# Performance work log

Hardware: AMD Instinct MI355X
Metric: run time of the kernel (lower is better)

## Reference

```python
import jax, jax.numpy as jnp
import numpy as np

B, S, D, H = 2, 2048, 1024, 16
DK = D // H  # 64


def setup_inputs() -> dict:
    key = jax.random.key(0)
    ks = jax.random.split(key, 9)
    s = 0.02
    return {
        "embeddings": jax.random.normal(ks[0], (B, S, D), jnp.float32),
        "Wq": jax.random.normal(ks[1], (H, D, DK), jnp.float32) * s,
        "bq": jax.random.normal(ks[2], (H, DK), jnp.float32) * s,
        "Wk": jax.random.normal(ks[3], (H, D, DK), jnp.float32) * s,
        "bk": jax.random.normal(ks[4], (H, DK), jnp.float32) * s,
        "Wv": jax.random.normal(ks[5], (H, D, DK), jnp.float32) * s,
        "bv": jax.random.normal(ks[6], (H, DK), jnp.float32) * s,
        "Wo": jax.random.normal(ks[7], (D, D), jnp.float32) * s,
        "bo": jax.random.normal(ks[8], (D,), jnp.float32) * s,
    }


def reference(embeddings, Wq, bq, Wk, bk, Wv, bv, Wo, bo):
    b, s, d = embeddings.shape
    dk = Wq.shape[-1]
    # batched per-head projections: [b,s,d] x [h,d,k] -> [b,h,s,k]
    q = jnp.einsum('bsd,hdk->bhsk', embeddings, Wq) + bq[None, :, None, :]
    k = jnp.einsum('bsd,hdk->bhsk', embeddings, Wk) + bk[None, :, None, :]
    v = jnp.einsum('bsd,hdk->bhsk', embeddings, Wv) + bv[None, :, None, :]
    scores = jnp.einsum('bhqk,bhsk->bhqs', q, k) / jnp.sqrt(jnp.float32(dk))
    causal_mask = jnp.triu(jnp.ones((s, s), dtype=bool), k=1)  # True above diagonal
    scores = jnp.where(causal_mask, jnp.float32(-1e9), scores)
    weights = jax.nn.softmax(scores, axis=-1)
    ctx = jnp.einsum('bhqs,bhsk->bhqk', weights, v)
    concat = ctx.transpose(0, 2, 1, 3).reshape(b, s, d)  # head-major concat, matches torch.cat
    return concat @ Wo + bo
```

## Files before the change

### kernel.cpp

```cpp
#include <hip/hip_runtime.h>
#include <hip/hip_bf16.h>

typedef unsigned short u16;
typedef unsigned int u32;
typedef __bf16 bf16x8 __attribute__((ext_vector_type(8)));
typedef float f32x4 __attribute__((ext_vector_type(4)));
typedef float f32x16 __attribute__((ext_vector_type(16)));

#define AS1 __attribute__((address_space(1)))
#define AS3 __attribute__((address_space(3)))

#define NB 2
#define NS 2048
#define ND 1024
#define NH 16
#define NK 64

__device__ __forceinline__ u16 f2bf(float f) {
  u32 u = __builtin_bit_cast(u32, f);
  return (u16)((u + 0x7FFFu + ((u >> 16) & 1u)) >> 16);
}

__device__ __forceinline__ u32 cvt_pk_bf16(float lo, float hi) {
  u32 u;
  asm("v_cvt_pk_bf16_f32 %0, %1, %2" : "=v"(u) : "v"(lo), "v"(hi));
  return u;
}

__device__ __forceinline__ void stage_tile(u16* lds, const u16* __restrict__ src, int rs,
                                           int wid, int lane) {
#pragma unroll
  for (int i = 0; i < 2; ++i) {
    int c = wid * 128 + i * 64 + lane;
    int row = c >> 3;
    int kc = (c & 7) ^ (row & 7);
    __builtin_amdgcn_global_load_lds((const AS1 u32*)(src + row * rs + kc * 8),
                                     (AS3 u32*)(lds + (wid * 128 + i * 64) * 8), 16, 0, 0);
  }
}

__device__ __forceinline__ bf16x8 read_slot(const u16* lds, int row, int slot) {
  return *(const bf16x8*)(lds + row * 64 + (slot ^ (row & 7)) * 8);
}

__device__ __forceinline__ uint2 ld8(const u16* lds, int row, int col) {
  int slot = (col >> 3) ^ (row & 7);
  return *(const uint2*)(lds + row * 64 + slot * 8 + (col & 7));
}

__device__ __forceinline__ bf16x8 read_vfrag(const u16* lds, int row, int ks, int hi) {
  int c0 = ks * 16 + 4 * hi;
  uint2 a = ld8(lds, row, c0);
  uint2 b = ld8(lds, row, c0 + 8);
  uint4 q; q.x = a.x; q.y = a.y; q.z = b.x; q.w = b.y;
  return __builtin_bit_cast(bf16x8, q);
}

__device__ __forceinline__ bf16x8 read_frag(const u16* lds, int row, int ks, int lane) {
  int slot = ((lane >> 4) + ks * 4) ^ (row & 7);
  return *(const bf16x8*)(lds + row * 64 + slot * 8);
}

__global__ __launch_bounds__(256) void convert_kernel(const float* __restrict__ src,
                                                      u16* __restrict__ dst, int n) {
  int i = (blockIdx.x * 256 + threadIdx.x) * 4;
  if (i >= n) return;
  float4 v = *(const float4*)(src + i);
  u32 w0 = cvt_pk_bf16(v.x, v.y);
  u32 w1 = cvt_pk_bf16(v.z, v.w);
  uint2 w; w.x = w0; w.y = w1;
  *(uint2*)(dst + i) = w;
}

__global__ __launch_bounds__(256) void transpose_conv(const float* __restrict__ src,
                                                      u16* __restrict__ dst, int R, int C) {
  __shared__ float tile[32][33];
  size_t base = (size_t)blockIdx.z * R * C;
  src += base;
  dst += base;
  int c0 = blockIdx.x * 32, r0 = blockIdx.y * 32;
  int tx = threadIdx.x, ty = threadIdx.y;
#pragma unroll
  for (int i = 0; i < 4; ++i)
    tile[ty + 8 * i][tx] = src[(size_t)(r0 + ty + 8 * i) * C + c0 + tx];
  __syncthreads();
#pragma unroll
  for (int i = 0; i < 4; ++i)
    dst[(size_t)(c0 + ty + 8 * i) * R + r0 + tx] = f2bf(tile[tx][ty + 8 * i]);
}

__global__ __launch_bounds__(256) void qkv_kernel(
    const u16* __restrict__ emb, const u16* __restrict__ Wqt, const u16* __restrict__ Wkt,
    const u16* __restrict__ Wvt, const float* __restrict__ bq, const float* __restrict__ bk,
    const float* __restrict__ bv, u16* __restrict__ Q, u16* __restrict__ K,
    u16* __restrict__ Vt) {
  __shared__ alignas(16) u16 lds_a[64 * 64];
  __shared__ alignas(16) u16 lds_b[64 * 64];
  int tid = threadIdx.x, lane = tid & 63, wid = tid >> 6;
  int mt = blockIdx.x, h = blockIdx.y, which = blockIdx.z;
  const u16* Wt = (which == 0 ? Wqt : which == 1 ? Wkt : Wvt) + h * (ND * NK);
  const float* bias = (which == 0 ? bq : which == 1 ? bk : bv) + h * NK;
  int m0 = mt * 64;
  int col = lane & 15;
  f32x4 zero4 = {0.f, 0.f, 0.f, 0.f};
  f32x4 acc[4] = {zero4, zero4, zero4, zero4};
  for (int k0 = 0; k0 < ND; k0 += 64) {
    stage_tile(lds_a, emb + m0 * ND + k0, ND, wid, lane);
    stage_tile(lds_b, Wt + k0, ND, wid, lane);
    __syncthreads();
#pragma unroll
    for (int ks = 0; ks < 2; ++ks) {
      bf16x8 a = read_frag(lds_a, wid * 16 + col, ks, lane);
#pragma unroll
      for (int f = 0; f < 4; ++f) {
        bf16x8 b = read_frag(lds_b, f * 16 + col, ks, lane);
        acc[f] = __builtin_amdgcn_mfma_f32_16x16x32_bf16(a, b, acc[f], 0, 0, 0);
      }
    }
    __syncthreads();
  }
  int rbase = m0 + wid * 16 + (lane >> 4) * 4;
#pragma unroll
  for (int f = 0; f < 4; ++f) {
    int n = f * 16 + col;
    float bn = bias[n];
#pragma unroll
    for (int r = 0; r < 4; ++r) {
      int m = rbase + r;
      int b = m >> 11, s = m & (NS - 1);
      float v = acc[f][r] + bn;
      if (which == 0) {
        Q[((b * NH + h) * NS + s) * NK + n] = f2bf(v * 0.18033688f);
      } else if (which == 1) {
        K[((b * NH + h) * NS + s) * NK + n] = f2bf(v);
      } else {
        Vt[((b * NH + h) * NK + n) * NS + s] = f2bf(v);
      }
    }
  }
}

__global__ __launch_bounds__(256, 2) void attn_kernel(const u16* __restrict__ Q,
                                                      const u16* __restrict__ K,
                                                      const u16* __restrict__ Vt,
                                                      u16* __restrict__ ctx) {
  __shared__ alignas(16) u16 lds_k[2][64 * 64];
  __shared__ alignas(16) u16 lds_v[2][64 * 64];
  __shared__ float slab[4][32];
  int tid = threadIdx.x, lane = tid & 63, w = tid >> 6;
  int hi = lane >> 5, ln = lane & 31;
  int bh = blockIdx.x;
  int y = blockIdx.y;
  int qt = (y < 8) ? (15 - y) : (y - 8);
  const u16* Qb = Q + bh * (NS * NK);
  const u16* Kb = K + bh * (NS * NK);
  const u16* Vb = Vt + bh * (NK * NS);
  int q0w = qt * 128 + w * 32;
  int qg = q0w + ln;
  bf16x8 qf[4];
#pragma unroll
  for (int ks = 0; ks < 4; ++ks)
    qf[ks] = *(const bf16x8*)(Qb + qg * NK + ks * 16 + hi * 8);

  f32x16 acc0, acc1;
#pragma unroll
  for (int r = 0; r < 16; ++r) { acc0[r] = 0.f; acc1[r] = 0.f; }
  float m = -1e30f, lp = 0.f;
  int nt = 2 * qt + 2;
  int tmaxw = (q0w + 31) >> 6;

  stage_tile(lds_k[0], Kb, NK, w, lane);
  stage_tile(lds_v[0], Vb, NS, w, lane);
  __syncthreads();

  for (int t = 0; t < nt; ++t) {
    int cur = t & 1;
    if (t + 1 < nt) {
      stage_tile(lds_k[cur ^ 1], Kb + (t + 1) * 64 * NK, NK, w, lane);
      stage_tile(lds_v[cur ^ 1], Vb + (t + 1) * 64, NS, w, lane);
    }
    if (t <= tmaxw) {
      const u16* lk = lds_k[cur];
      const u16* lv = lds_v[cur];
      f32x16 sc0, sc1;
#pragma unroll
      for (int r = 0; r < 16; ++r) { sc0[r] = 0.f; sc1[r] = 0.f; }
      __builtin_amdgcn_s_setprio(1);
#pragma unroll
      for (int ks = 0; ks < 4; ++ks) {
        bf16x8 kf0 = read_slot(lk, ln, 2 * ks + hi);
        sc0 = __builtin_amdgcn_mfma_f32_32x32x16_bf16(kf0, qf[ks], sc0, 0, 0, 0);
        bf16x8 kf1 = read_slot(lk, 32 + ln, 2 * ks + hi);
        sc1 = __builtin_amdgcn_mfma_f32_32x32x16_bf16(kf1, qf[ks], sc1, 0, 0, 0);
      }
      __builtin_amdgcn_s_setprio(0);
      if (t == tmaxw) {
#pragma unroll
        for (int r = 0; r < 16; ++r) {
          int kl = t * 64 + (r & 3) + 8 * (r >> 2) + 4 * hi;
          if (kl > qg) sc0[r] = -1e30f;
          if (kl + 32 > qg) sc1[r] = -1e30f;
        }
      }
      float mt_[16];
#pragma unroll
      for (int i = 0; i < 16; ++i) mt_[i] = fmaxf(sc0[i], sc1[i]);
#pragma unroll
      for (int s = 8; s > 0; s >>= 1)
#pragma unroll
        for (int i = 0; i < s; ++i) mt_[i] = fmaxf(mt_[i], mt_[i + s]);
      float mx = mt_[0];
      mx = fmaxf(mx, __shfl_xor(mx, 32));
      if (__any(mx > m + 8.0f)) {
        float mn = fmaxf(m, mx);
        float al = exp2f(m - mn);
        m = mn;
        lp *= al;
        if (!hi) slab[w][ln] = al;
        float av[16];
#pragma unroll
        for (int r = 0; r < 16; ++r) av[r] = slab[w][(r & 3) + 8 * (r >> 2) + 4 * hi];
#pragma unroll
        for (int r = 0; r < 16; ++r) { acc0[r] *= av[r]; acc1[r] *= av[r]; }
      }
      float ps[4] = {0.f, 0.f, 0.f, 0.f};
#pragma unroll
      for (int r = 0; r < 16; ++r) {
        float p = exp2f(sc0[r] - m);
        sc0[r] = p;
        ps[r & 3] += p;
      }
#pragma unroll
      for (int r = 0; r < 16; ++r) {
        float p = exp2f(sc1[r] - m);
        sc1[r] = p;
        ps[r & 3] += p;
      }
      lp += (ps[0] + ps[1]) + (ps[2] + ps[3]);
      u32 wd[8];
      bf16x8 pa[4];
#pragma unroll
      for (int i = 0; i < 8; ++i) wd[i] = cvt_pk_bf16(sc0[2 * i], sc0[2 * i + 1]);
      { uint4 q4; q4.x = wd[0]; q4.y = wd[1]; q4.z = wd[2]; q4.w = wd[3];
        pa[0] = __builtin_bit_cast(bf16x8, q4);
        q4.x = wd[4]; q4.y = wd[5]; q4.z = wd[6]; q4.w = wd[7];
        pa[1] = __builtin_bit_cast(bf16x8, q4); }
#pragma unroll
      for (int i = 0; i < 8; ++i) wd[i] = cvt_pk_bf16(sc1[2 * i], sc1[2 * i + 1]);
      { uint4 q4; q4.x = wd[0]; q4.y = wd[1]; q4.z = wd[2]; q4.w = wd[3];
        pa[2] = __builtin_bit_cast(bf16x8, q4);
        q4.x = wd[4]; q4.y = wd[5]; q4.z = wd[6]; q4.w = wd[7];
        pa[3] = __builtin_bit_cast(bf16x8, q4); }
      __builtin_amdgcn_s_setprio(1);
#pragma unroll
      for (int ks = 0; ks < 4; ++ks) {
        bf16x8 vf0 = read_vfrag(lv, ln, ks, hi);
        acc0 = __builtin_amdgcn_mfma_f32_32x32x16_bf16(pa[ks], vf0, acc0, 0, 0, 0);
        bf16x8 vf1 = read_vfrag(lv, 32 + ln, ks, hi);
        acc1 = __builtin_amdgcn_mfma_f32_32x32x16_bf16(pa[ks], vf1, acc1, 0, 0, 0);
      }
      __builtin_amdgcn_s_setprio(0);
    }
    __syncthreads();
  }
  lp += __shfl_xor(lp, 32);
  if (!hi) slab[w][ln] = 1.0f / lp;
  float iv[16];
#pragma unroll
  for (int r = 0; r < 16; ++r) iv[r] = slab[w][(r & 3) + 8 * (r >> 2) + 4 * hi];
  int b = bh >> 4, h = bh & 15;
#pragma unroll
  for (int r = 0; r < 16; ++r) {
    int qq = q0w + (r & 3) + 8 * (r >> 2) + 4 * hi;
    size_t base = (size_t)(b * NS + qq) * ND + h * NK + ln;
    ctx[base] = f2bf(acc0[r] * iv[r]);
    ctx[base + 32] = f2bf(acc1[r] * iv[r]);
  }
}

__global__ __launch_bounds__(256) void outproj_kernel(const u16* __restrict__ ctx,
                                                      const u16* __restrict__ Wot,
                                                      const float* __restrict__ bo,
                                                      float* __restrict__ out) {
  __shared__ alignas(16) u16 lds_a[64 * 64];
  __shared__ alignas(16) u16 lds_b[64 * 64];
  int tid = threadIdx.x, lane = tid & 63, wid = tid >> 6;
  int m0 = blockIdx.x * 64, n0 = blockIdx.y * 64;
  int col = lane & 15;
  f32x4 zero4 = {0.f, 0.f, 0.f, 0.f};
  f32x4 acc[4] = {zero4, zero4, zero4, zero4};
  for (int k0 = 0; k0 < ND; k0 += 64) {
    stage_tile(lds_a, ctx + m0 * ND + k0, ND, wid, lane);
    stage_tile(lds_b, Wot + n0 * ND + k0, ND, wid, lane);
    __syncthreads();
#pragma unroll
    for (int ks = 0; ks < 2; ++ks) {
      bf16x8 a = read_frag(lds_a, wid * 16 + col, ks, lane);
#pragma unroll
      for (int f = 0; f < 4; ++f) {
        bf16x8 b = read_frag(lds_b, f * 16 + col, ks, lane);
        acc[f] = __builtin_amdgcn_mfma_f32_16x16x32_bf16(a, b, acc[f], 0, 0, 0);
      }
    }
    __syncthreads();
  }
  int rbase = m0 + wid * 16 + (lane >> 4) * 4;
#pragma unroll
  for (int f = 0; f < 4; ++f) {
    int n = n0 + f * 16 + col;
    float bn = bo[n];
#pragma unroll
    for (int r = 0; r < 4; ++r) out[(rbase + r) * ND + n] = acc[f][r] + bn;
  }
}

extern "C" void kernel_launch(void* const* d_in, const int* in_sizes, int n_in,
                              void* d_out, int out_size, void* d_ws, size_t ws_size,
                              hipStream_t stream) {
  (void)in_sizes; (void)n_in; (void)out_size;
  const float* emb = (const float*)d_in[0];
  const float* Wq = (const float*)d_in[1];
  const float* bq = (const float*)d_in[2];
  const float* Wk = (const float*)d_in[3];
  const float* bk = (const float*)d_in[4];
  const float* Wv = (const float*)d_in[5];
  const float* bv = (const float*)d_in[6];
  const float* Wo = (const float*)d_in[7];
  const float* bo = (const float*)d_in[8];
  float* out = (float*)d_out;

  const size_t EMB_N = (size_t)NB * NS * ND;
  const size_t W_N = (size_t)NH * ND * NK;
  const size_t QKV_N = (size_t)NB * NH * NS * NK;
  if (ws_size < (EMB_N + 4 * W_N + 3 * QKV_N) * sizeof(u16)) return;
  u16* ws = (u16*)d_ws;
  u16* emb_bf = ws;
  u16* Wqt = emb_bf + EMB_N;
  u16* Wkt = Wqt + W_N;
  u16* Wvt = Wkt + W_N;
  u16* Wot = Wvt + W_N;
  u16* Qb = Wot + W_N;
  u16* Kb = Qb + QKV_N;
  u16* Vtb = Kb + QKV_N;
  u16* ctxb = emb_bf;

  convert_kernel<<<dim3((int)(EMB_N / 4 / 256)), dim3(256), 0, stream>>>(emb, emb_bf,
                                                                         (int)EMB_N);
  dim3 tb(32, 8);
  transpose_conv<<<dim3(2, 32, 16), tb, 0, stream>>>(Wq, Wqt, ND, NK);
  transpose_conv<<<dim3(2, 32, 16), tb, 0, stream>>>(Wk, Wkt, ND, NK);
  transpose_conv<<<dim3(2, 32, 16), tb, 0, stream>>>(Wv, Wvt, ND, NK);
  transpose_conv<<<dim3(32, 32, 1), tb, 0, stream>>>(Wo, Wot, ND, ND);
  qkv_kernel<<<dim3(64, 16, 3), dim3(256), 0, stream>>>(emb_bf, Wqt, Wkt, Wvt, bq, bk, bv,
                                                        Qb, Kb, Vtb);
  attn_kernel<<<dim3(32, 16), dim3(256), 0, stream>>>(Qb, Kb, Vtb, ctxb);
  outproj_kernel<<<dim3(64, 16), dim3(256), 0, stream>>>(ctxb, Wot, bo, out);
}
```

Before: 138.4 us.

## Use 128x128 GEMM tiles for projections and pair causal q-tiles per attention block

```diff
diff --git a/kernel.cpp b/kernel.cpp
--- a/kernel.cpp
+++ b/kernel.cpp
@@ -34,7 +34,7 @@
     int c = wid * 128 + i * 64 + lane;
     int row = c >> 3;
     int kc = (c & 7) ^ (row & 7);
-    __builtin_amdgcn_global_load_lds((const AS1 u32*)(src + row * rs + kc * 8),
+    __builtin_amdgcn_global_load_lds((const AS1 u32*)(src + (size_t)row * rs + kc * 8),
                                      (AS3 u32*)(lds + (wid * 128 + i * 64) * 8), 16, 0, 0);
   }
 }
@@ -89,53 +89,92 @@
     dst[(size_t)(c0 + ty + 8 * i) * R + r0 + tx] = f2bf(tile[tx][ty + 8 * i]);
 }
 
-__global__ __launch_bounds__(256) void qkv_kernel(
-    const u16* __restrict__ emb, const u16* __restrict__ Wqt, const u16* __restrict__ Wkt,
-    const u16* __restrict__ Wvt, const float* __restrict__ bq, const float* __restrict__ bk,
-    const float* __restrict__ bv, u16* __restrict__ Q, u16* __restrict__ K,
-    u16* __restrict__ Vt) {
-  __shared__ alignas(16) u16 lds_a[64 * 64];
-  __shared__ alignas(16) u16 lds_b[64 * 64];
+template <int MODE>
+__global__ __launch_bounds__(256) void gemm128(const u16* __restrict__ A,
+                                               const u16* __restrict__ Bt,
+                                               const float* __restrict__ b0,
+                                               const float* __restrict__ b1,
+                                               const float* __restrict__ b2,
+                                               u16* __restrict__ Qo, u16* __restrict__ Ko,
+                                               u16* __restrict__ Vo,
+                                               float* __restrict__ out) {
+  __shared__ alignas(16) u16 lds_a[128 * 64];
+  __shared__ alignas(16) u16 lds_b[128 * 64];
   int tid = threadIdx.x, lane = tid & 63, wid = tid >> 6;
-  int mt = blockIdx.x, h = blockIdx.y, which = blockIdx.z;
-  const u16* Wt = (which == 0 ? Wqt : which == 1 ? Wkt : Wvt) + h * (ND * NK);
-  const float* bias = (which == 0 ? bq : which == 1 ? bk : bv) + h * NK;
-  int m0 = mt * 64;
+  int wm = wid >> 1, wn = wid & 1;
+  int m0 = blockIdx.x * 128, n0 = blockIdx.y * 128;
   int col = lane & 15;
   f32x4 zero4 = {0.f, 0.f, 0.f, 0.f};
-  f32x4 acc[4] = {zero4, zero4, zero4, zero4};
+  f32x4 acc[4][4];
+#pragma unroll
+  for (int i = 0; i < 4; ++i)
+#pragma unroll
+    for (int j = 0; j < 4; ++j) acc[i][j] = zero4;
   for (int k0 = 0; k0 < ND; k0 += 64) {
-    stage_tile(lds_a, emb + m0 * ND + k0, ND, wid, lane);
-    stage_tile(lds_b, Wt + k0, ND, wid, lane);
+    stage_tile(lds_a, A + (size_t)m0 * ND + k0, ND, wid, lane);
+    stage_tile(lds_a + 4096, A + (size_t)(m0 + 64) * ND + k0, ND, wid, lane);
+    stage_tile(lds_b, Bt + (size_t)n0 * ND + k0, ND, wid, lane);
+    stage_tile(lds_b + 4096, Bt + (size_t)(n0 + 64) * ND + k0, ND, wid, lane);
     __syncthreads();
 #pragma unroll
     for (int ks = 0; ks < 2; ++ks) {
-      bf16x8 a = read_frag(lds_a, wid * 16 + col, ks, lane);
-#pragma unroll
-      for (int f = 0; f < 4; ++f) {
-        bf16x8 b = read_frag(lds_b, f * 16 + col, ks, lane);
-        acc[f] = __builtin_amdgcn_mfma_f32_16x16x32_bf16(a, b, acc[f], 0, 0, 0);
-      }
+      bf16x8 af[4], bf[4];
+#pragma unroll
+      for (int i = 0; i < 4; ++i) af[i] = read_frag(lds_a, wm * 64 + i * 16 + col, ks, lane);
+#pragma unroll
+      for (int j = 0; j < 4; ++j) bf[j] = read_frag(lds_b, wn * 64 + j * 16 + col, ks, lane);
+#pragma unroll
+      for (int i = 0; i < 4; ++i)
+#pragma unroll
+        for (int j = 0; j < 4; ++j)
+          acc[i][j] = __builtin_amdgcn_mfma_f32_16x16x32_bf16(af[i], bf[j], acc[i][j], 0, 0, 0);
     }
     __syncthreads();
   }
-  int rbase = m0 + wid * 16 + (lane >> 4) * 4;
-#pragma unroll
-  for (int f = 0; f < 4; ++f) {
-    int n = f * 16 + col;
-    float bn = bias[n];
-#pragma unroll
-    for (int r = 0; r < 4; ++r) {
-      int m = rbase + r;
-      int b = m >> 11, s = m & (NS - 1);
-      float v = acc[f][r] + bn;
+  int rbase = m0 + wm * 64 + (lane >> 4) * 4;
+#pragma unroll
+  for (int j = 0; j < 4; ++j) {
+    int n = n0 + wn * 64 + j * 16 + col;
+    if constexpr (MODE == 0) {
+      int which = n >> 10, hh = (n >> 6) & 15, dk = n & 63;
+      const float* bp = which == 0 ? b0 : which == 1 ? b1 : b2;
+      float bn = bp[hh * 64 + dk];
       if (which == 0) {
-        Q[((b * NH + h) * NS + s) * NK + n] = f2bf(v * 0.18033688f);
+#pragma unroll
+        for (int i = 0; i < 4; ++i)
+#pragma unroll
+          for (int r = 0; r < 4; ++r) {
+            int m = rbase + i * 16 + r;
+            int bb = m >> 11, s = m & (NS - 1);
+            Qo[((size_t)(bb * NH + hh) * NS + s) * NK + dk] =
+                f2bf((acc[i][j][r] + bn) * 0.18033688f);
+          }
       } else if (which == 1) {
-        K[((b * NH + h) * NS + s) * NK + n] = f2bf(v);
+#pragma unroll
+        for (int i = 0; i < 4; ++i)
+#pragma unroll
+          for (int r = 0; r < 4; ++r) {
+            int m = rbase + i * 16 + r;
+            int bb = m >> 11, s = m & (NS - 1);
+            Ko[((size_t)(bb * NH + hh) * NS + s) * NK + dk] = f2bf(acc[i][j][r] + bn);
+          }
       } else {
-        Vt[((b * NH + h) * NK + n) * NS + s] = f2bf(v);
+#pragma unroll
+        for (int i = 0; i < 4; ++i)
+#pragma unroll
+          for (int r = 0; r < 4; ++r) {
+            int m = rbase + i * 16 + r;
+            int bb = m >> 11, s = m & (NS - 1);
+            Vo[((size_t)(bb * NH + hh) * NK + dk) * NS + s] = f2bf(acc[i][j][r] + bn);
+          }
       }
+    } else {
+      float bn = b0[n];
+#pragma unroll
+      for (int i = 0; i < 4; ++i)
+#pragma unroll
+        for (int r = 0; r < 4; ++r)
+          out[(size_t)(rbase + i * 16 + r) * ND + n] = acc[i][j][r] + bn;
     }
   }
 }
@@ -150,167 +189,135 @@
   int tid = threadIdx.x, lane = tid & 63, w = tid >> 6;
   int hi = lane >> 5, ln = lane & 31;
   int bh = blockIdx.x;
-  int y = blockIdx.y;
-  int qt = (y < 8) ? (15 - y) : (y - 8);
+  int pr = blockIdx.y;
   const u16* Qb = Q + bh * (NS * NK);
   const u16* Kb = K + bh * (NS * NK);
   const u16* Vb = Vt + bh * (NK * NS);
-  int q0w = qt * 128 + w * 32;
-  int qg = q0w + ln;
-  bf16x8 qf[4];
-#pragma unroll
-  for (int ks = 0; ks < 4; ++ks)
-    qf[ks] = *(const bf16x8*)(Qb + qg * NK + ks * 16 + hi * 8);
-
-  f32x16 acc0, acc1;
-#pragma unroll
-  for (int r = 0; r < 16; ++r) { acc0[r] = 0.f; acc1[r] = 0.f; }
-  float m = -1e30f, lp = 0.f;
-  int nt = 2 * qt + 2;
-  int tmaxw = (q0w + 31) >> 6;
-
-  stage_tile(lds_k[0], Kb, NK, w, lane);
-  stage_tile(lds_v[0], Vb, NS, w, lane);
-  __syncthreads();
-
-  for (int t = 0; t < nt; ++t) {
-    int cur = t & 1;
-    if (t + 1 < nt) {
-      stage_tile(lds_k[cur ^ 1], Kb + (t + 1) * 64 * NK, NK, w, lane);
-      stage_tile(lds_v[cur ^ 1], Vb + (t + 1) * 64, NS, w, lane);
+  int b = bh >> 4, h = bh & 15;
+
+#pragma unroll 1
+  for (int half = 0; half < 2; ++half) {
+    int qt = half ? pr : (15 - pr);
+    int q0w = qt * 128 + w * 32;
+    int qg = q0w + ln;
+    bf16x8 qf[4];
+#pragma unroll
+    for (int ks = 0; ks < 4; ++ks)
+      qf[ks] = *(const bf16x8*)(Qb + qg * NK + ks * 16 + hi * 8);
+
+    f32x16 acc0, acc1;
+#pragma unroll
+    for (int r = 0; r < 16; ++r) { acc0[r] = 0.f; acc1[r] = 0.f; }
+    float m = -1e30f, lp = 0.f;
+    int nt = 2 * qt + 2;
+    int tmaxw = (q0w + 31) >> 6;
+
+    stage_tile(lds_k[0], Kb, NK, w, lane);
+    stage_tile(lds_v[0], Vb, NS, w, lane);
+    __syncthreads();
+
+    for (int t = 0; t < nt; ++t) {
+      int cur = t & 1;
+      if (t + 1 < nt) {
+        stage_tile(lds_k[cur ^ 1], Kb + (t + 1) * 64 * NK, NK, w, lane);
+        stage_tile(lds_v[cur ^ 1], Vb + (t + 1) * 64, NS, w, lane);
+      }
+      if (t <= tmaxw) {
+        const u16* lk = lds_k[cur];
+        const u16* lv = lds_v[cur];
+        f32x16 sc0, sc1;
+#pragma unroll
+        for (int r = 0; r < 16; ++r) { sc0[r] = 0.f; sc1[r] = 0.f; }
+        __builtin_amdgcn_s_setprio(1);
+#pragma unroll
+        for (int ks = 0; ks < 4; ++ks) {
+          bf16x8 kf0 = read_slot(lk, ln, 2 * ks + hi);
+          sc0 = __builtin_amdgcn_mfma_f32_32x32x16_bf16(kf0, qf[ks], sc0, 0, 0, 0);
+          bf16x8 kf1 = read_slot(lk, 32 + ln, 2 * ks + hi);
+          sc1 = __builtin_amdgcn_mfma_f32_32x32x16_bf16(kf1, qf[ks], sc1, 0, 0, 0);
+        }
+        __builtin_amdgcn_s_setprio(0);
+        if (t == tmaxw) {
+#pragma unroll
+          for (int r = 0; r < 16; ++r) {
+            int kl = t * 64 + (r & 3) + 8 * (r >> 2) + 4 * hi;
+            if (kl > qg) sc0[r] = -1e30f;
+            if (kl + 32 > qg) sc1[r] = -1e30f;
+          }
+        }
+        float mt_[16];
+#pragma unroll
+        for (int i = 0; i < 16; ++i) mt_[i] = fmaxf(sc0[i], sc1[i]);
+#pragma unroll
+        for (int s = 8; s > 0; s >>= 1)
+#pragma unroll
+          for (int i = 0; i < s; ++i) mt_[i] = fmaxf(mt_[i], mt_[i + s]);
+        float mx = mt_[0];
+        mx = fmaxf(mx, __shfl_xor(mx, 32));
+        if (__any(mx > m + 8.0f)) {
+          float mn = fmaxf(m, mx);
+          float al = exp2f(m - mn);
+          m = mn;
+          lp *= al;
+          if (!hi) slab[w][ln] = al;
+          float av[16];
+#pragma unroll
+          for (int r = 0; r < 16; ++r) av[r] = slab[w][(r & 3) + 8 * (r >> 2) + 4 * hi];
+#pragma unroll
+          for (int r = 0; r < 16; ++r) { acc0[r] *= av[r]; acc1[r] *= av[r]; }
+        }
+        float ps[4] = {0.f, 0.f, 0.f, 0.f};
+#pragma unroll
+        for (int r = 0; r < 16; ++r) {
+          float p = exp2f(sc0[r] - m);
+          sc0[r] = p;
+          ps[r & 3] += p;
+        }
+#pragma unroll
+        for (int r = 0; r < 16; ++r) {
+          float p = exp2f(sc1[r] - m);
+          sc1[r] = p;
+          ps[r & 3] += p;
+        }
+        lp += (ps[0] + ps[1]) + (ps[2] + ps[3]);
+        u32 wd[8];
+        bf16x8 pa[4];
+#pragma unroll
+        for (int i = 0; i < 8; ++i) wd[i] = cvt_pk_bf16(sc0[2 * i], sc0[2 * i + 1]);
+        { uint4 q4; q4.x = wd[0]; q4.y = wd[1]; q4.z = wd[2]; q4.w = wd[3];
+          pa[0] = __builtin_bit_cast(bf16x8, q4);
+          q4.x = wd[4]; q4.y = wd[5]; q4.z = wd[6]; q4.w = wd[7];
+          pa[1] = __builtin_bit_cast(bf16x8, q4); }
+#pragma unroll
+        for (int i = 0; i < 8; ++i) wd[i] = cvt_pk_bf16(sc1[2 * i], sc1[2 * i + 1]);
+        { uint4 q4; q4.x = wd[0]; q4.y = wd[1]; q4.z = wd[2]; q4.w = wd[3];
+          pa[2] = __builtin_bit_cast(bf16x8, q4);
+          q4.x = wd[4]; q4.y = wd[5]; q4.z = wd[6]; q4.w = wd[7];
+          pa[3] = __builtin_bit_cast(bf16x8, q4); }
+        __builtin_amdgcn_s_setprio(1);
+#pragma unroll
+        for (int ks = 0; ks < 4; ++ks) {
+          bf16x8 vf0 = read_vfrag(lv, ln, ks, hi);
+          acc0 = __builtin_amdgcn_mfma_f32_32x32x16_bf16(pa[ks], vf0, acc0, 0, 0, 0);
+          bf16x8 vf1 = read_vfrag(lv, 32 + ln, ks, hi);
+          acc1 = __builtin_amdgcn_mfma_f32_32x32x16_bf16(pa[ks], vf1, acc1, 0, 0, 0);
+        }
+        __builtin_amdgcn_s_setprio(0);
+      }
+      __syncthreads();
     }
-    if (t <= tmaxw) {
-      const u16* lk = lds_k[cur];
-      const u16* lv = lds_v[cur];
-      f32x16 sc0, sc1;
-#pragma unroll
-      for (int r = 0; r < 16; ++r) { sc0[r] = 0.f; sc1[r] = 0.f; }
-      __builtin_amdgcn_s_setprio(1);
-#pragma unroll
-      for (int ks = 0; ks < 4; ++ks) {
-        bf16x8 kf0 = read_slot(lk, ln, 2 * ks + hi);
-        sc0 = __builtin_amdgcn_mfma_f32_32x32x16_bf16(kf0, qf[ks], sc0, 0, 0, 0);
-        bf16x8 kf1 = read_slot(lk, 32 + ln, 2 * ks + hi);
-        sc1 = __builtin_amdgcn_mfma_f32_32x32x16_bf16(kf1, qf[ks], sc1, 0, 0, 0);
-      }
-      __builtin_amdgcn_s_setprio(0);
-      if (t == tmaxw) {
-#pragma unroll
-        for (int r = 0; r < 16; ++r) {
-          int kl = t * 64 + (r & 3) + 8 * (r >> 2) + 4 * hi;
-          if (kl > qg) sc0[r] = -1e30f;
-          if (kl + 32 > qg) sc1[r] = -1e30f;
-        }
-      }
-      float mt_[16];
-#pragma unroll
-      for (int i = 0; i < 16; ++i) mt_[i] = fmaxf(sc0[i], sc1[i]);
-#pragma unroll
-      for (int s = 8; s > 0; s >>= 1)
-#pragma unroll
-        for (int i = 0; i < s; ++i) mt_[i] = fmaxf(mt_[i], mt_[i + s]);
-      float mx = mt_[0];
-      mx = fmaxf(mx, __shfl_xor(mx, 32));
-      if (__any(mx > m + 8.0f)) {
-        float mn = fmaxf(m, mx);
-        float al = exp2f(m - mn);
-        m = mn;
-        lp *= al;
-        if (!hi) slab[w][ln] = al;
-        float av[16];
-#pragma unroll
-        for (int r = 0; r < 16; ++r) av[r] = slab[w][(r & 3) + 8 * (r >> 2) + 4 * hi];
-#pragma unroll
-        for (int r = 0; r < 16; ++r) { acc0[r] *= av[r]; acc1[r] *= av[r]; }
-      }
-      float ps[4] = {0.f, 0.f, 0.f, 0.f};
-#pragma unroll
-      for (int r = 0; r < 16; ++r) {
-        float p = exp2f(sc0[r] - m);
-        sc0[r] = p;
-        ps[r & 3] += p;
-      }
-#pragma unroll
-      for (int r = 0; r < 16; ++r) {
-        float p = exp2f(sc1[r] - m);
-        sc1[r] = p;
-        ps[r & 3] += p;
-      }
-      lp += (ps[0] + ps[1]) + (ps[2] + ps[3]);
-      u32 wd[8];
-      bf16x8 pa[4];
-#pragma unroll
-      for (int i = 0; i < 8; ++i) wd[i] = cvt_pk_bf16(sc0[2 * i], sc0[2 * i + 1]);
-      { uint4 q4; q4.x = wd[0]; q4.y = wd[1]; q4.z = wd[2]; q4.w = wd[3];
-        pa[0] = __builtin_bit_cast(bf16x8, q4);
-        q4.x = wd[4]; q4.y = wd[5]; q4.z = wd[6]; q4.w = wd[7];
-        pa[1] = __builtin_bit_cast(bf16x8, q4); }
-#pragma unroll
-      for (int i = 0; i < 8; ++i) wd[i] = cvt_pk_bf16(sc1[2 * i], sc1[2 * i + 1]);
-      { uint4 q4; q4.x = wd[0]; q4.y = wd[1]; q4.z = wd[2]; q4.w = wd[3];
-        pa[2] = __builtin_bit_cast(bf16x8, q4);
-        q4.x = wd[4]; q4.y = wd[5]; q4.z = wd[6]; q4.w = wd[7];
-        pa[3] = __builtin_bit_cast(bf16x8, q4); }
-      __builtin_amdgcn_s_setprio(1);
-#pragma unroll
-      for (int ks = 0; ks < 4; ++ks) {
-        bf16x8 vf0 = read_vfrag(lv, ln, ks, hi);
-        acc0 = __builtin_amdgcn_mfma_f32_32x32x16_bf16(pa[ks], vf0, acc0, 0, 0, 0);
-        bf16x8 vf1 = read_vfrag(lv, 32 + ln, ks, hi);
-        acc1 = __builtin_amdgcn_mfma_f32_32x32x16_bf16(pa[ks], vf1, acc1, 0, 0, 0);
-      }
-      __builtin_amdgcn_s_setprio(0);
+    lp += __shfl_xor(lp, 32);
+    if (!hi) slab[w][ln] = 1.0f / lp;
+    float iv[16];
+#pragma unroll
+    for (int r = 0; r < 16; ++r) iv[r] = slab[w][(r & 3) + 8 * (r >> 2) + 4 * hi];
+#pragma unroll
+    for (int r = 0; r < 16; ++r) {
+      int qq = q0w + (r & 3) + 8 * (r >> 2) + 4 * hi;
+      size_t base = (size_t)(b * NS + qq) * ND + h * NK + ln;
+      ctx[base] = f2bf(acc0[r] * iv[r]);
+      ctx[base + 32] = f2bf(acc1[r] * iv[r]);
     }
-    __syncthreads();
-  }
-  lp += __shfl_xor(lp, 32);
-  if (!hi) slab[w][ln] = 1.0f / lp;
-  float iv[16];
-#pragma unroll
-  for (int r = 0; r < 16; ++r) iv[r] = slab[w][(r & 3) + 8 * (r >> 2) + 4 * hi];
-  int b = bh >> 4, h = bh & 15;
-#pragma unroll
-  for (int r = 0; r < 16; ++r) {
-    int qq = q0w + (r & 3) + 8 * (r >> 2) + 4 * hi;
-    size_t base = (size_t)(b * NS + qq) * ND + h * NK + ln;
-    ctx[base] = f2bf(acc0[r] * iv[r]);
-    ctx[base + 32] = f2bf(acc1[r] * iv[r]);
-  }
-}
-
-__global__ __launch_bounds__(256) void outproj_kernel(const u16* __restrict__ ctx,
-                                                      const u16* __restrict__ Wot,
-                                                      const float* __restrict__ bo,
-                                                      float* __restrict__ out) {
-  __shared__ alignas(16) u16 lds_a[64 * 64];
-  __shared__ alignas(16) u16 lds_b[64 * 64];
-  int tid = threadIdx.x, lane = tid & 63, wid = tid >> 6;
-  int m0 = blockIdx.x * 64, n0 = blockIdx.y * 64;
-  int col = lane & 15;
-  f32x4 zero4 = {0.f, 0.f, 0.f, 0.f};
-  f32x4 acc[4] = {zero4, zero4, zero4, zero4};
-  for (int k0 = 0; k0 < ND; k0 += 64) {
-    stage_tile(lds_a, ctx + m0 * ND + k0, ND, wid, lane);
-    stage_tile(lds_b, Wot + n0 * ND + k0, ND, wid, lane);
-    __syncthreads();
-#pragma unroll
-    for (int ks = 0; ks < 2; ++ks) {
-      bf16x8 a = read_frag(lds_a, wid * 16 + col, ks, lane);
-#pragma unroll
-      for (int f = 0; f < 4; ++f) {
-        bf16x8 b = read_frag(lds_b, f * 16 + col, ks, lane);
-        acc[f] = __builtin_amdgcn_mfma_f32_16x16x32_bf16(a, b, acc[f], 0, 0, 0);
-      }
-    }
-    __syncthreads();
-  }
-  int rbase = m0 + wid * 16 + (lane >> 4) * 4;
-#pragma unroll
-  for (int f = 0; f < 4; ++f) {
-    int n = n0 + f * 16 + col;
-    float bn = bo[n];
-#pragma unroll
-    for (int r = 0; r < 4; ++r) out[(rbase + r) * ND + n] = acc[f][r] + bn;
   }
 }
 
@@ -351,8 +358,9 @@
   transpose_conv<<<dim3(2, 32, 16), tb, 0, stream>>>(Wk, Wkt, ND, NK);
   transpose_conv<<<dim3(2, 32, 16), tb, 0, stream>>>(Wv, Wvt, ND, NK);
   transpose_conv<<<dim3(32, 32, 1), tb, 0, stream>>>(Wo, Wot, ND, ND);
-  qkv_kernel<<<dim3(64, 16, 3), dim3(256), 0, stream>>>(emb_bf, Wqt, Wkt, Wvt, bq, bk, bv,
-                                                        Qb, Kb, Vtb);
-  attn_kernel<<<dim3(32, 16), dim3(256), 0, stream>>>(Qb, Kb, Vtb, ctxb);
-  outproj_kernel<<<dim3(64, 16), dim3(256), 0, stream>>>(ctxb, Wot, bo, out);
-}
+  gemm128<0><<<dim3(32, 24), dim3(256), 0, stream>>>(emb_bf, Wqt, bq, bk, bv, Qb, Kb, Vtb,
+                                                     nullptr);
+  attn_kernel<<<dim3(32, 8), dim3(256), 0, stream>>>(Qb, Kb, Vtb, ctxb);
+  gemm128<1><<<dim3(32, 8), dim3(256), 0, stream>>>(ctxb, Wot, bo, nullptr, nullptr,
+                                                    nullptr, nullptr, nullptr, out);
+}
```

After: 148.1 us. 1.07x slower.
